# Kernel optimization log

Hardware: AMD Instinct MI355X
Metric: run time of the kernel (lower is better)

Reference implementation:

```python
import jax, jax.numpy as jnp
import numpy as np

B, S, UNITS = 32, 4096, 512

def setup_inputs() -> dict:
    key = jax.random.key(0)
    ks = jax.random.split(key, 5)
    scale = 1.0 / np.sqrt(UNITS)
    return {
        "s_prev": jax.random.normal(ks[0], (B, UNITS), dtype=jnp.float32),
        "hidden_states": jax.random.normal(ks[1], (B, S, UNITS), dtype=jnp.float32),
        "Ww": jax.random.normal(ks[2], (UNITS, UNITS), dtype=jnp.float32) * scale,
        "Wb": jnp.zeros((UNITS,), dtype=jnp.float32),
        "Uw": jax.random.normal(ks[3], (UNITS, UNITS), dtype=jnp.float32) * scale,
        "Ub": jnp.zeros((UNITS,), dtype=jnp.float32),
        "Vw": jax.random.normal(ks[4], (UNITS, 1), dtype=jnp.float32) * scale,
        "Vb": jnp.zeros((1,), dtype=jnp.float32),
    }

def reference(s_prev, hidden_states, Ww, Wb, Uw, Ub, Vw, Vb):
    # W(s_prev): [B, 1, U] so it broadcasts over seq axis
    W_s = (s_prev @ Ww + Wb)[:, None, :]
    # U(hidden_states): [B, S, U]
    U_h = jnp.einsum('bsu,uv->bsv', hidden_states, Uw) + Ub
    score = jnp.tanh(W_s + U_h)                      # [B, S, U]
    logits = jnp.einsum('bsu,uo->bso', score, Vw) + Vb  # [B, S, 1]
    weights = jax.nn.softmax(logits, axis=1)         # softmax over seq axis
    context = jnp.sum(weights * hidden_states, axis=1)  # [B, U]
    return (context, weights)
```

## Files before the change

### kernel.cpp

```cpp
#include <hip/hip_runtime.h>
#include <hip/hip_bf16.h>

#define UNITS 512
#define SEQ   4096
#define BATCH 32

typedef __attribute__((ext_vector_type(8))) __bf16 bf16x8;
typedef __attribute__((ext_vector_type(4))) float  f32x4;

__device__ __forceinline__ int swz(int l) { return l ^ (((l >> 6) & 7) << 4); }

__global__ void k_bprep(const float* __restrict__ Uw, __bf16* __restrict__ UwTt) {
    const int c     = blockIdx.x;
    const int half  = blockIdx.y;
    const int kstep = blockIdx.z;
    const int t     = threadIdx.x;
    const int n = half * 256 + t;
    bf16x8 o;
#pragma unroll
    for (int j = 0; j < 8; j++)
        o[j] = (__bf16)Uw[(size_t)(kstep * 32 + c * 8 + j) * UNITS + n];
    const int tile = kstep * 2 + half;
    char* dst = (char*)UwTt + (size_t)tile * 16384 + swz(t * 64 + c * 16);
    *(bf16x8*)dst = o;
}

__global__ void k_wsrow(const float* __restrict__ s_prev, const float* __restrict__ Ww,
                        const float* __restrict__ Wb, const float* __restrict__ Ub,
                        float* __restrict__ ws_Ws) {
    __shared__ float sp[UNITS];
    int b = blockIdx.x, t = threadIdx.x;
    sp[t] = s_prev[b * UNITS + t];
    sp[t + 256] = s_prev[b * UNITS + t + 256];
    __syncthreads();
    float a0 = Wb[t] + Ub[t];
    float a1 = Wb[t + 256] + Ub[t + 256];
#pragma unroll 8
    for (int u = 0; u < UNITS; u++) {
        float s = sp[u];
        a0 += s * Ww[u * UNITS + t];
        a1 += s * Ww[u * UNITS + t + 256];
    }
    ws_Ws[b * UNITS + t] = a0;
    ws_Ws[b * UNITS + t + 256] = a1;
}

#define BM 128
#define BN 256
#define BK 32
#define NSTEP (UNITS / BK)

__launch_bounds__(512, 4)
__global__ void k_logits(const float* __restrict__ hidden, const __bf16* __restrict__ UwTt,
                         const float* __restrict__ wsu, const float* __restrict__ Vw,
                         float* __restrict__ lpart) {
    __shared__ __bf16 Ab[2][BM * BK];
    __shared__ __bf16 Bb[2][BN * BK];
    __shared__ float  lred[BM][4];

    const int t = threadIdx.x;
    const int lane = t & 63, wv = t >> 6;
    const int wm = wv >> 2, wn = wv & 3;
    const int l15 = lane & 15, l4 = lane >> 4;
    const int gx = blockIdx.x;
    const int m0 = blockIdx.y * BM;
    const int b  = m0 >> 12;

    f32x4 acc[4][4];
#pragma unroll
    for (int i = 0; i < 4; i++)
#pragma unroll
        for (int j = 0; j < 4; j++) acc[i][j] = (f32x4){0.f, 0.f, 0.f, 0.f};

    const int sr = t >> 2;
    const int sc = t & 3;
    const float* aRow = hidden + (size_t)(m0 + sr) * UNITS + sc * 8;
    const int aoffW = swz(sr * 64 + sc * 16);

    int aoffR[4], boffR[4];
#pragma unroll
    for (int f = 0; f < 4; f++) {
        aoffR[f] = swz((wm * 64 + f * 16 + l15) * 64 + l4 * 16);
        boffR[f] = swz((wn * 64 + f * 16 + l15) * 64 + l4 * 16);
    }

    auto issueA = [&](float4& v0, float4& v1, int kk) {
        v0 = *(const float4*)(aRow + kk);
        v1 = *(const float4*)(aRow + kk + 4);
    };
    auto issueB = [&](int buf, int step) {
        const char* src = (const char*)UwTt + (size_t)(step * 2 + gx) * 16384
                        + wv * 2048 + lane * 16;
        char* dst = (char*)(&Bb[buf][0]) + wv * 2048;
        __builtin_amdgcn_global_load_lds(
            (const __attribute__((address_space(1))) void*)src,
            (__attribute__((address_space(3))) void*)dst, 16, 0, 0);
        __builtin_amdgcn_global_load_lds(
            (const __attribute__((address_space(1))) void*)(src + 1024),
            (__attribute__((address_space(3))) void*)(dst + 1024), 16, 0, 0);
    };

    float4 ev0, ev1, ov0, ov1;

    issueA(ev0, ev1, 0);  issueB(0, 0);
    issueA(ov0, ov1, BK); issueB(1, 1);

    auto body = [&](int s, int cur, float4& v0, float4& v1, bool last) {
        bf16x8 o;
        o[0] = (__bf16)v0.x; o[1] = (__bf16)v0.y; o[2] = (__bf16)v0.z; o[3] = (__bf16)v0.w;
        o[4] = (__bf16)v1.x; o[5] = (__bf16)v1.y; o[6] = (__bf16)v1.z; o[7] = (__bf16)v1.w;
        *(bf16x8*)((char*)(&Ab[cur][0]) + aoffW) = o;
        if (last) asm volatile("s_waitcnt vmcnt(0) lgkmcnt(0)" ::: "memory");
        else      asm volatile("s_waitcnt vmcnt(4) lgkmcnt(0)" ::: "memory");
        __builtin_amdgcn_s_barrier();

        bf16x8 a[4], bq[4];
#pragma unroll
        for (int fi = 0; fi < 4; fi++)
            a[fi] = *(const bf16x8*)((char*)(&Ab[cur][0]) + aoffR[fi]);
#pragma unroll
        for (int fj = 0; fj < 4; fj++)
            bq[fj] = *(const bf16x8*)((char*)(&Bb[cur][0]) + boffR[fj]);
        __builtin_amdgcn_s_setprio(1);
#pragma unroll
        for (int fi = 0; fi < 4; fi++)
#pragma unroll
            for (int fj = 0; fj < 4; fj++)
                acc[fi][fj] = __builtin_amdgcn_mfma_f32_16x16x32_bf16(a[fi], bq[fj], acc[fi][fj], 0, 0, 0);
        __builtin_amdgcn_s_setprio(0);
        asm volatile("s_waitcnt lgkmcnt(0)" ::: "memory");
        __builtin_amdgcn_s_barrier();
        __builtin_amdgcn_sched_barrier(0);
        if (s + 2 < NSTEP) {
            issueA(v0, v1, (s + 2) * BK);
            issueB(cur, s + 2);
        }
    };

    for (int i = 0; i < 7; i++) {
        body(2 * i,     0, ev0, ev1, false);
        body(2 * i + 1, 1, ov0, ov1, false);
    }
    body(14, 0, ev0, ev1, false);
    body(15, 1, ov0, ov1, true);

    float wsub[4], vww[4];
#pragma unroll
    for (int fj = 0; fj < 4; fj++) {
        int n = gx * BN + wn * 64 + fj * 16 + l15;
        wsub[fj] = wsu[b * UNITS + n];
        vww[fj]  = Vw[n];
    }
#pragma unroll
    for (int fi = 0; fi < 4; fi++) {
#pragma unroll
        for (int r = 0; r < 4; r++) {
            float p = 0.f;
#pragma unroll
            for (int fj = 0; fj < 4; fj++) {
                float x = acc[fi][fj][r] + wsub[fj];
                float e = __expf(2.f * x);
                p += vww[fj] * (1.f - 2.f / (e + 1.f));
            }
#pragma unroll
            for (int off = 1; off < 16; off <<= 1) p += __shfl_xor(p, off);
            if (l15 == 0) lred[wm * 64 + fi * 16 + l4 * 4 + r][wn] = p;
        }
    }
    __syncthreads();
    if (t < BM) {
        float s = lred[t][0] + lred[t][1] + lred[t][2] + lred[t][3];
        lpart[(size_t)(m0 + t) * 2 + gx] = s;
    }
}

__global__ void k_softmax(const float* __restrict__ lpart, float* __restrict__ wout) {
    __shared__ float ebuf[SEQ];
    __shared__ float red[8];
    int b = blockIdx.x, t = threadIdx.x;
    int lane = t & 63, wv = t >> 6;
    float m = -1e30f;
#pragma unroll
    for (int i = 0; i < 16; i++) {
        int s = t + i * 256;
        size_t idx = ((size_t)b * SEQ + s) * 2;
        float l = lpart[idx] + lpart[idx + 1];
        ebuf[s] = l;
        m = fmaxf(m, l);
    }
#pragma unroll
    for (int off = 32; off >= 1; off >>= 1) m = fmaxf(m, __shfl_xor(m, off));
    if (lane == 0) red[wv] = m;
    __syncthreads();
    m = fmaxf(fmaxf(red[0], red[1]), fmaxf(red[2], red[3]));
    float zs = 0.f;
#pragma unroll
    for (int i = 0; i < 16; i++) {
        int s = t + i * 256;
        float e = __expf(ebuf[s] - m);
        ebuf[s] = e;
        zs += e;
    }
#pragma unroll
    for (int off = 32; off >= 1; off >>= 1) zs += __shfl_xor(zs, off);
    __syncthreads();
    if (lane == 0) red[wv] = zs;
    __syncthreads();
    float inv = 1.f / (red[0] + red[1] + red[2] + red[3]);
#pragma unroll
    for (int i = 0; i < 16; i++) {
        int s = t + i * 256;
        wout[(size_t)b * SEQ + s] = ebuf[s] * inv;
    }
}

__global__ void k_ctxpart(const float* __restrict__ hidden, const float* __restrict__ wout,
                          float* __restrict__ part) {
    int b = blockIdx.y, c = blockIdx.x, t = threadIdx.x;
    const float* w = wout + (size_t)b * SEQ + c * 128;
    const float* h = hidden + ((size_t)b * SEQ + c * 128) * UNITS;
    float2 acc = make_float2(0.f, 0.f);
#pragma unroll 4
    for (int s = 0; s < 128; s++) {
        float ww = w[s];
        float2 v = ((const float2*)(h + (size_t)s * UNITS))[t];
        acc.x += ww * v.x;
        acc.y += ww * v.y;
    }
    ((float2*)(part + ((size_t)(b * 32 + c)) * UNITS))[t] = acc;
}

__global__ void k_ctxreduce(const float* __restrict__ part, float* __restrict__ ctx) {
    int b = blockIdx.x, t = threadIdx.x;
    float s = 0.f;
#pragma unroll
    for (int c = 0; c < 32; c++) s += part[((size_t)(b * 32 + c)) * UNITS + t];
    ctx[(size_t)b * UNITS + t] = s;
}

extern "C" void kernel_launch(void* const* d_in, const int* in_sizes, int n_in,
                              void* d_out, int out_size, void* d_ws, size_t ws_size,
                              hipStream_t stream) {
    const float* s_prev = (const float*)d_in[0];
    const float* hidden = (const float*)d_in[1];
    const float* Ww     = (const float*)d_in[2];
    const float* Wb     = (const float*)d_in[3];
    const float* Uw     = (const float*)d_in[4];
    const float* Ub     = (const float*)d_in[5];
    const float* Vw     = (const float*)d_in[6];

    float* out  = (float*)d_out;
    float* ctx  = out;
    float* wout = out + BATCH * UNITS;

    float* wsf   = (float*)d_ws;
    float* ws_Ws = wsf;
    float* ws_lp = ws_Ws + BATCH * UNITS;
    float* ws_cp = ws_lp + (size_t)BATCH * SEQ * 2;
    __bf16* UwTt = (__bf16*)(ws_cp + (size_t)BATCH * 32 * UNITS);

    k_bprep<<<dim3(4, 2, 16), dim3(256), 0, stream>>>(Uw, UwTt);
    k_wsrow<<<dim3(32), dim3(256), 0, stream>>>(s_prev, Ww, Wb, Ub, ws_Ws);
    k_logits<<<dim3(2, 1024), dim3(512), 0, stream>>>(hidden, UwTt, ws_Ws, Vw, ws_lp);
    k_softmax<<<dim3(32), dim3(256), 0, stream>>>(ws_lp, wout);
    k_ctxpart<<<dim3(32, 32), dim3(256), 0, stream>>>(hidden, wout, ws_cp);
    k_ctxreduce<<<dim3(32), dim3(512), 0, stream>>>(ws_cp, ctx);
}
```

Measured before the change: 243.4 us.

## Stream fp32 A tiles into LDS with direct global-to-LDS loads

The hidden-state (A) tile is now copied as fp32 straight into LDS with global_load_lds, the same way the B tile already was. This replaces the register staging and the convert-then-store path, and uses a new swizzle sized for 128-byte rows. The bf16 conversion moves to after the LDS read, so each wave converts its own fragments redundantly. The aim is to remove VGPR pressure and the ds_write on the load path and make prefetch fully asynchronous. In exchange, the A buffers double in LDS size, which may lower occupancy, and conversion ALU work increases.

```diff
diff --git a/kernel.cpp b/kernel.cpp
--- a/kernel.cpp
+++ b/kernel.cpp
@@ -8,7 +8,8 @@
 typedef __attribute__((ext_vector_type(8))) __bf16 bf16x8;
 typedef __attribute__((ext_vector_type(4))) float  f32x4;
 
-__device__ __forceinline__ int swz(int l) { return l ^ (((l >> 6) & 7) << 4); }
+__device__ __forceinline__ int swzB(int l) { return l ^ (((l >> 6) & 7) << 4); }
+__device__ __forceinline__ int swzA(int l) { return l ^ (((l >> 7) & 7) << 4); }
 
 __global__ void k_bprep(const float* __restrict__ Uw, __bf16* __restrict__ UwTt) {
     const int c     = blockIdx.x;
@@ -21,7 +22,7 @@
     for (int j = 0; j < 8; j++)
         o[j] = (__bf16)Uw[(size_t)(kstep * 32 + c * 8 + j) * UNITS + n];
     const int tile = kstep * 2 + half;
-    char* dst = (char*)UwTt + (size_t)tile * 16384 + swz(t * 64 + c * 16);
+    char* dst = (char*)UwTt + (size_t)tile * 16384 + swzB(t * 64 + c * 16);
     *(bf16x8*)dst = o;
 }
 
@@ -54,7 +55,7 @@
 __global__ void k_logits(const float* __restrict__ hidden, const __bf16* __restrict__ UwTt,
                          const float* __restrict__ wsu, const float* __restrict__ Vw,
                          float* __restrict__ lpart) {
-    __shared__ __bf16 Ab[2][BM * BK];
+    __shared__ float  Af[2][BM * BK];
     __shared__ __bf16 Bb[2][BN * BK];
     __shared__ float  lred[BM][4];
 
@@ -72,55 +73,67 @@
 #pragma unroll
         for (int j = 0; j < 4; j++) acc[i][j] = (f32x4){0.f, 0.f, 0.f, 0.f};
 
-    const int sr = t >> 2;
-    const int sc = t & 3;
-    const float* aRow = hidden + (size_t)(m0 + sr) * UNITS + sc * 8;
-    const int aoffW = swz(sr * 64 + sc * 16);
+    const int aphys0 = wv * 2048 + lane * 16;
+    const int alog0  = swzA(aphys0);
+    const int arow0  = alog0 >> 7;
+    const int acolb  = alog0 & 127;
+    const char* asrc0 = (const char*)(hidden + (size_t)(m0 + arow0) * UNITS) + acolb;
+    const char* asrc1 = (const char*)(hidden + (size_t)(m0 + arow0 + 8) * UNITS) + acolb;
 
     int aoffR[4], boffR[4];
 #pragma unroll
     for (int f = 0; f < 4; f++) {
-        aoffR[f] = swz((wm * 64 + f * 16 + l15) * 64 + l4 * 16);
-        boffR[f] = swz((wn * 64 + f * 16 + l15) * 64 + l4 * 16);
-    }
-
-    auto issueA = [&](float4& v0, float4& v1, int kk) {
-        v0 = *(const float4*)(aRow + kk);
-        v1 = *(const float4*)(aRow + kk + 4);
+        aoffR[f] = swzA((wm * 64 + f * 16 + l15) * 128 + l4 * 32);
+        boffR[f] = swzB((wn * 64 + f * 16 + l15) * 64 + l4 * 16);
+    }
+
+    auto issue = [&](int buf, int s) {
+        char* adst = (char*)(&Af[buf][0]) + wv * 2048;
+        __builtin_amdgcn_global_load_lds(
+            (const __attribute__((address_space(1))) void*)(asrc0 + s * 128),
+            (__attribute__((address_space(3))) void*)adst, 16, 0, 0);
+        __builtin_amdgcn_global_load_lds(
+            (const __attribute__((address_space(1))) void*)(asrc1 + s * 128),
+            (__attribute__((address_space(3))) void*)(adst + 1024), 16, 0, 0);
+        const char* bsrc = (const char*)UwTt + (size_t)(s * 2 + gx) * 16384
+                         + wv * 2048 + lane * 16;
+        char* bdst = (char*)(&Bb[buf][0]) + wv * 2048;
+        __builtin_amdgcn_global_load_lds(
+            (const __attribute__((address_space(1))) void*)bsrc,
+            (__attribute__((address_space(3))) void*)bdst, 16, 0, 0);
+        __builtin_amdgcn_global_load_lds(
+            (const __attribute__((address_space(1))) void*)(bsrc + 1024),
+            (__attribute__((address_space(3))) void*)(bdst + 1024), 16, 0, 0);
     };
-    auto issueB = [&](int buf, int step) {
-        const char* src = (const char*)UwTt + (size_t)(step * 2 + gx) * 16384
-                        + wv * 2048 + lane * 16;
-        char* dst = (char*)(&Bb[buf][0]) + wv * 2048;
-        __builtin_amdgcn_global_load_lds(
-            (const __attribute__((address_space(1))) void*)src,
-            (__attribute__((address_space(3))) void*)dst, 16, 0, 0);
-        __builtin_amdgcn_global_load_lds(
-            (const __attribute__((address_space(1))) void*)(src + 1024),
-            (__attribute__((address_space(3))) void*)(dst + 1024), 16, 0, 0);
-    };
-
-    float4 ev0, ev1, ov0, ov1;
-
-    issueA(ev0, ev1, 0);  issueB(0, 0);
-    issueA(ov0, ov1, BK); issueB(1, 1);
-
-    auto body = [&](int s, int cur, float4& v0, float4& v1, bool last) {
-        bf16x8 o;
-        o[0] = (__bf16)v0.x; o[1] = (__bf16)v0.y; o[2] = (__bf16)v0.z; o[3] = (__bf16)v0.w;
-        o[4] = (__bf16)v1.x; o[5] = (__bf16)v1.y; o[6] = (__bf16)v1.z; o[7] = (__bf16)v1.w;
-        *(bf16x8*)((char*)(&Ab[cur][0]) + aoffW) = o;
-        if (last) asm volatile("s_waitcnt vmcnt(0) lgkmcnt(0)" ::: "memory");
-        else      asm volatile("s_waitcnt vmcnt(4) lgkmcnt(0)" ::: "memory");
+
+    issue(0, 0);
+    issue(1, 1);
+
+#pragma unroll
+    for (int s = 0; s < NSTEP; ++s) {
+        const int cur = s & 1;
+        if (s < NSTEP - 1) asm volatile("s_waitcnt vmcnt(4)" ::: "memory");
+        else               asm volatile("s_waitcnt vmcnt(0)" ::: "memory");
         __builtin_amdgcn_s_barrier();
 
         bf16x8 a[4], bq[4];
 #pragma unroll
-        for (int fi = 0; fi < 4; fi++)
-            a[fi] = *(const bf16x8*)((char*)(&Ab[cur][0]) + aoffR[fi]);
+        for (int fi = 0; fi < 4; fi++) {
+            f32x4 r0 = *(const f32x4*)((const char*)(&Af[cur][0]) + aoffR[fi]);
+            f32x4 r1 = *(const f32x4*)((const char*)(&Af[cur][0]) + (aoffR[fi] ^ 16));
+            bf16x8 av;
+            av[0] = (__bf16)r0[0]; av[1] = (__bf16)r0[1];
+            av[2] = (__bf16)r0[2]; av[3] = (__bf16)r0[3];
+            av[4] = (__bf16)r1[0]; av[5] = (__bf16)r1[1];
+            av[6] = (__bf16)r1[2]; av[7] = (__bf16)r1[3];
+            a[fi] = av;
+        }
 #pragma unroll
         for (int fj = 0; fj < 4; fj++)
-            bq[fj] = *(const bf16x8*)((char*)(&Bb[cur][0]) + boffR[fj]);
+            bq[fj] = *(const bf16x8*)((const char*)(&Bb[cur][0]) + boffR[fj]);
+
+        asm volatile("s_waitcnt lgkmcnt(0)" ::: "memory");
+        __builtin_amdgcn_sched_barrier(0);
         __builtin_amdgcn_s_setprio(1);
 #pragma unroll
         for (int fi = 0; fi < 4; fi++)
@@ -128,21 +141,9 @@
             for (int fj = 0; fj < 4; fj++)
                 acc[fi][fj] = __builtin_amdgcn_mfma_f32_16x16x32_bf16(a[fi], bq[fj], acc[fi][fj], 0, 0, 0);
         __builtin_amdgcn_s_setprio(0);
-        asm volatile("s_waitcnt lgkmcnt(0)" ::: "memory");
         __builtin_amdgcn_s_barrier();
-        __builtin_amdgcn_sched_barrier(0);
-        if (s + 2 < NSTEP) {
-            issueA(v0, v1, (s + 2) * BK);
-            issueB(cur, s + 2);
-        }
-    };
-
-    for (int i = 0; i < 7; i++) {
-        body(2 * i,     0, ev0, ev1, false);
-        body(2 * i + 1, 1, ov0, ov1, false);
-    }
-    body(14, 0, ev0, ev1, false);
-    body(15, 1, ov0, ov1, true);
+        if (s + 2 < NSTEP) issue(cur, s + 2);
+    }
 
     float wsub[4], vww[4];
 #pragma unroll
```

After: 211.4 us. 13.1% less time.
